# Kernel optimization log

Measured on AMD Instinct MI355X. Metric: run time of the kernel, lower is better.

The kernel has to match this reference:

```python
import jax, jax.numpy as jnp
import numpy as np

D_MODEL = 1024
NUM_HEADS = 16
D_K = D_MODEL // NUM_HEADS


def setup_inputs() -> dict:
    key = jax.random.key(0)
    ks = jax.random.split(key, 12)
    B, S = 2, 2048
    s = 1.0 / np.sqrt(D_MODEL)
    return {
        "Q": jax.random.normal(ks[0], (B, S, D_MODEL), jnp.float32),
        "K": jax.random.normal(ks[1], (B, S, D_MODEL), jnp.float32),
        "V": jax.random.normal(ks[2], (B, S, D_MODEL), jnp.float32),
        "Wq": jax.random.normal(ks[3], (D_MODEL, D_MODEL), jnp.float32) * s,
        "bq": jax.random.normal(ks[4], (D_MODEL,), jnp.float32) * s,
        "Wk": jax.random.normal(ks[5], (D_MODEL, D_MODEL), jnp.float32) * s,
        "bk": jax.random.normal(ks[6], (D_MODEL,), jnp.float32) * s,
        "Wv": jax.random.normal(ks[7], (D_MODEL, D_MODEL), jnp.float32) * s,
        "bv": jax.random.normal(ks[8], (D_MODEL,), jnp.float32) * s,
        "Wfc": jax.random.normal(ks[9], (D_MODEL, D_MODEL), jnp.float32) * s,
        "bfc": jax.random.normal(ks[10], (D_MODEL,), jnp.float32) * s,
    }


def reference(Q, K, V, Wq, bq, Wk, bk, Wv, bv, Wfc, bfc):
    B, S, _ = Q.shape
    # Linear projections, then split heads: [B, S, D] -> [B, H, S, d_k]
    def split_heads(x):
        return x.reshape(B, S, NUM_HEADS, D_K).transpose(0, 2, 1, 3)
    q = split_heads(Q @ Wq + bq)
    k = split_heads(K @ Wk + bk)
    v = split_heads(V @ Wv + bv)
    # Scaled dot-product attention (mask=None path)
    scores = jnp.einsum('bhqd,bhkd->bhqk', q, k) / jnp.sqrt(jnp.asarray(D_K, q.dtype))
    attention = jax.nn.softmax(scores, axis=-1)  # [B, H, S, S]
    context = jnp.einsum('bhqk,bhkd->bhqd', attention, v)
    context = context.transpose(0, 2, 1, 3).reshape(B, S, D_MODEL)
    output = context @ Wfc + bfc
    return output, attention
```

## Files before the change

### kernel.cpp

```cpp
#include <hip/hip_runtime.h>
#include <hip/hip_bf16.h>
#include <stdint.h>


typedef __bf16 bf16_t;
typedef __bf16 bf16x8 __attribute__((ext_vector_type(8)));
typedef float  f32x4  __attribute__((ext_vector_type(4)));

#define MFMA16(a, b, c) __builtin_amdgcn_mfma_f32_16x16x32_bf16((a), (b), (c), 0, 0, 0)

__global__ __launch_bounds__(256)
void wtrans_kernel(const float* w0, const float* w1, const float* w2,
                   const float* w3, bf16_t* wt)
{
  const float* W = blockIdx.z == 0 ? w0 : blockIdx.z == 1 ? w1
                 : blockIdx.z == 2 ? w2 : w3;
  bf16_t* O = wt + ((size_t)blockIdx.z << 20);
  __shared__ bf16_t tile[64][72];
  const int t = threadIdx.x;
  const int r0 = blockIdx.y * 64, c0 = blockIdx.x * 64;
  {
    const int r = t >> 2, cg = (t & 3) * 16;
    const float4* src = (const float4*)(W + (size_t)(r0 + r) * 1024 + c0 + cg);
#pragma unroll
    for (int u = 0; u < 4; ++u) {
      float4 f = src[u];
      tile[r][cg + u * 4 + 0] = (bf16_t)f.x;
      tile[r][cg + u * 4 + 1] = (bf16_t)f.y;
      tile[r][cg + u * 4 + 2] = (bf16_t)f.z;
      tile[r][cg + u * 4 + 3] = (bf16_t)f.w;
    }
  }
  __syncthreads();
  {
    const int c = t >> 2, rg = (t & 3) * 16;
    bf16x8 v0, v1;
#pragma unroll
    for (int u = 0; u < 8; ++u) { v0[u] = tile[rg + u][c]; v1[u] = tile[rg + 8 + u][c]; }
    bf16x8* dst = (bf16x8*)(O + (size_t)(c0 + c) * 1024 + r0 + rg);
    dst[0] = v0; dst[1] = v1;
  }
}

__global__ __launch_bounds__(256)
void vtrans_kernel(const bf16_t* vb, bf16_t* vT)
{
  __shared__ bf16_t tile[64][72];
  const int t = threadIdx.x;
  const int bh = blockIdx.y;
  const int s0 = blockIdx.x * 64;
  {
    const int s = t >> 2, dg = (t & 3) * 16;
    const bf16x8* src = (const bf16x8*)(vb + ((size_t)bh * 2048 + s0 + s) * 64 + dg);
    bf16x8 a = src[0], b = src[1];
#pragma unroll
    for (int u = 0; u < 8; ++u) { tile[s][dg + u] = a[u]; tile[s][dg + 8 + u] = b[u]; }
  }
  __syncthreads();
  {
    const int d = t >> 2, sg = (t & 3) * 16;
    bf16x8 v0, v1;
#pragma unroll
    for (int u = 0; u < 8; ++u) { v0[u] = tile[sg + u][d]; v1[u] = tile[sg + 8 + u][d]; }
    bf16x8* dst = (bf16x8*)(vT + ((size_t)bh * 64 + d) * 2048 + s0 + sg);
    dst[0] = v0; dst[1] = v1;
  }
}

template<bool A_BF16, bool OUT_SPLIT>
__global__ __launch_bounds__(256, 2)
void gemm_kernel(const void* A0, const void* A1, const void* A2,
                 const bf16_t* WTbase,
                 const float* b0, const float* b1, const float* b2,
                 void* Obase, size_t ostride)
{
  const int z = blockIdx.z;
  const void*  Aptr = z == 0 ? A0 : z == 1 ? A1 : A2;
  const float* bias = z == 0 ? b0 : z == 1 ? b1 : b2;
  const bf16_t* WT  = WTbase + ((size_t)z << 20);

  __shared__ bf16_t As[128 * 32];
  __shared__ bf16_t Bs[128 * 32];

  const int tid = threadIdx.x;
  const int lane = tid & 63, wv = tid >> 6;
  const int quad = lane >> 4, lr = lane & 15;
  const int wm = wv >> 1, wn = wv & 1;
  const int m0 = blockIdx.y * 128, n0 = blockIdx.x * 128;

  f32x4 acc[4][4];
#pragma unroll
  for (int i = 0; i < 4; ++i)
#pragma unroll
    for (int j = 0; j < 4; ++j) acc[i][j] = (f32x4){0.f, 0.f, 0.f, 0.f};

  const int srow = tid >> 1;
  const int shalf = tid & 1;
  const int swz = (srow >> 1) & 3;
  bf16_t* as0 = &As[srow * 32 + (((shalf * 2)    ) ^ swz) * 8];
  bf16_t* as1 = &As[srow * 32 + (((shalf * 2) + 1) ^ swz) * 8];
  bf16_t* bs0 = &Bs[srow * 32 + (((shalf * 2)    ) ^ swz) * 8];
  bf16_t* bs1 = &Bs[srow * 32 + (((shalf * 2) + 1) ^ swz) * 8];

  for (int kt = 0; kt < 1024; kt += 32) {
    bf16x8 av0, av1, bv0, bv1;
    if (A_BF16) {
      const bf16x8* p = (const bf16x8*)((const bf16_t*)Aptr +
                          (size_t)(m0 + srow) * 1024 + kt + shalf * 16);
      av0 = p[0]; av1 = p[1];
    } else {
      const float4* p = (const float4*)((const float*)Aptr +
                          (size_t)(m0 + srow) * 1024 + kt + shalf * 16);
      float4 f0 = p[0], f1 = p[1], f2 = p[2], f3 = p[3];
      av0[0]=(bf16_t)f0.x; av0[1]=(bf16_t)f0.y; av0[2]=(bf16_t)f0.z; av0[3]=(bf16_t)f0.w;
      av0[4]=(bf16_t)f1.x; av0[5]=(bf16_t)f1.y; av0[6]=(bf16_t)f1.z; av0[7]=(bf16_t)f1.w;
      av1[0]=(bf16_t)f2.x; av1[1]=(bf16_t)f2.y; av1[2]=(bf16_t)f2.z; av1[3]=(bf16_t)f2.w;
      av1[4]=(bf16_t)f3.x; av1[5]=(bf16_t)f3.y; av1[6]=(bf16_t)f3.z; av1[7]=(bf16_t)f3.w;
    }
    {
      const bf16x8* p = (const bf16x8*)(WT + (size_t)(n0 + srow) * 1024 + kt + shalf * 16);
      bv0 = p[0]; bv1 = p[1];
    }
    __syncthreads();
    *(bf16x8*)as0 = av0; *(bf16x8*)as1 = av1;
    *(bf16x8*)bs0 = bv0; *(bf16x8*)bs1 = bv1;
    __syncthreads();
    bf16x8 af[4], bfr[4];
#pragma unroll
    for (int i = 0; i < 4; ++i) {
      const int row = wm * 64 + i * 16 + lr;
      af[i] = *(bf16x8*)&As[row * 32 + (quad ^ ((row >> 1) & 3)) * 8];
      const int nn = wn * 64 + i * 16 + lr;
      bfr[i] = *(bf16x8*)&Bs[nn * 32 + (quad ^ ((nn >> 1) & 3)) * 8];
    }
#pragma unroll
    for (int i = 0; i < 4; ++i)
#pragma unroll
      for (int j = 0; j < 4; ++j)
        acc[i][j] = MFMA16(af[i], bfr[j], acc[i][j]);
  }

  if (OUT_SPLIT) {
    bf16_t* O = (bf16_t*)Obase + (size_t)z * ostride;
#pragma unroll
    for (int i = 0; i < 4; ++i) {
      const int mbase = m0 + wm * 64 + i * 16 + quad * 4;
#pragma unroll
      for (int j = 0; j < 4; ++j) {
        const int n = n0 + wn * 64 + j * 16 + lr;
        const float bv = bias[n];
        const int h = n >> 6, d = n & 63;
#pragma unroll
        for (int r = 0; r < 4; ++r) {
          const int m = mbase + r;
          const int b = m >> 11, s = m & 2047;
          O[((size_t)(b * 16 + h) * 2048 + s) * 64 + d] = (bf16_t)(acc[i][j][r] + bv);
        }
      }
    }
  } else {
    float* O = (float*)Obase;
#pragma unroll
    for (int i = 0; i < 4; ++i) {
      const int mbase = m0 + wm * 64 + i * 16 + quad * 4;
#pragma unroll
      for (int j = 0; j < 4; ++j) {
        const int n = n0 + wn * 64 + j * 16 + lr;
        const float bv = bias[n];
#pragma unroll
        for (int r = 0; r < 4; ++r)
          O[(size_t)(mbase + r) * 1024 + n] = acc[i][j][r] + bv;
      }
    }
  }
}

__global__ __launch_bounds__(256, 2)
void attn_kernel(const bf16_t* qb, const bf16_t* kb, const bf16_t* vT,
                 float* attn, bf16_t* ctx, float* wsum)
{
  __shared__ bf16_t P[16 * 2048];
  const int tid = threadIdx.x;
  const int lane = tid & 63, wv = tid >> 6;
  const int quad = lane >> 4, lr = lane & 15;
  const int bh = blockIdx.y;
  const int row0 = blockIdx.x * 16;
  const int blockflat = bh * 128 + blockIdx.x;

  const bf16x8* qp = (const bf16x8*)(qb + ((size_t)bh * 2048 + row0 + lr) * 64 + quad * 8);
  const bf16x8 a0 = qp[0];
  const bf16x8 a1 = qp[4];

  float sums[4] = {0.f, 0.f, 0.f, 0.f};

  for (int ct = 0; ct < 32; ++ct) {
    const int n0 = wv * 512 + ct * 16;
    const bf16x8* kp = (const bf16x8*)(kb + ((size_t)bh * 2048 + n0 + lr) * 64 + quad * 8);
    const bf16x8 b0v = kp[0];
    const bf16x8 b1v = kp[4];
    f32x4 sacc = {0.f, 0.f, 0.f, 0.f};
    sacc = MFMA16(a0, b0v, sacc);
    sacc = MFMA16(a1, b1v, sacc);
#pragma unroll
    for (int r = 0; r < 4; ++r) {
      const float p = __expf(sacc[r] * 0.125f);
      const bf16_t pb = (bf16_t)p;
      sums[r] += (float)pb;
      P[(quad * 4 + r) * 2048 + n0 + lr] = pb;
    }
  }
#pragma unroll
  for (int m = 1; m < 16; m <<= 1) {
#pragma unroll
    for (int r = 0; r < 4; ++r) sums[r] += __shfl_xor(sums[r], m, 64);
  }
  float* wsb = wsum + (size_t)blockflat * 64;
  if (lr == 0) {
#pragma unroll
    for (int r = 0; r < 4; ++r) wsb[wv * 16 + quad * 4 + r] = sums[r];
  }
  __syncthreads();

  {
    float* abase = attn + ((size_t)bh * 2048 + row0) * 2048 + tid * 8;
    for (int r = 0; r < 16; ++r) {
      const float inv = 1.0f / (wsb[r] + wsb[16 + r] + wsb[32 + r] + wsb[48 + r]);
      const bf16x8 pv = *(const bf16x8*)&P[r * 2048 + tid * 8];
      float4 o0, o1;
      o0.x = (float)pv[0] * inv; o0.y = (float)pv[1] * inv;
      o0.z = (float)pv[2] * inv; o0.w = (float)pv[3] * inv;
      o1.x = (float)pv[4] * inv; o1.y = (float)pv[5] * inv;
      o1.z = (float)pv[6] * inv; o1.w = (float)pv[7] * inv;
      float4* dst = (float4*)(abase + (size_t)r * 2048);
      dst[0] = o0; dst[1] = o1;
    }
  }

  {
    f32x4 cacc = {0.f, 0.f, 0.f, 0.f};
    const bf16_t* vbase = vT + ((size_t)bh * 64 + wv * 16 + lr) * 2048;
    for (int kt = 0; kt < 64; ++kt) {
      const bf16x8 af  = *(const bf16x8*)&P[lr * 2048 + kt * 32 + quad * 8];
      const bf16x8 bfv = *(const bf16x8*)(vbase + kt * 32 + quad * 8);
      cacc = MFMA16(af, bfv, cacc);
    }
    const int b = bh >> 4, h = bh & 15;
#pragma unroll
    for (int r = 0; r < 4; ++r) {
      const int row = quad * 4 + r;
      const float inv = 1.0f / (wsb[row] + wsb[16 + row] + wsb[32 + row] + wsb[48 + row]);
      ctx[(size_t)(b * 2048 + row0 + row) * 1024 + h * 64 + wv * 16 + lr] =
          (bf16_t)(cacc[r] * inv);
    }
  }
}

extern "C" void kernel_launch(void* const* d_in, const int* in_sizes, int n_in,
                              void* d_out, int out_size, void* d_ws, size_t ws_size,
                              hipStream_t stream)
{
  const float* Q   = (const float*)d_in[0];
  const float* K   = (const float*)d_in[1];
  const float* V   = (const float*)d_in[2];
  const float* Wq  = (const float*)d_in[3];
  const float* bq  = (const float*)d_in[4];
  const float* Wk  = (const float*)d_in[5];
  const float* bk  = (const float*)d_in[6];
  const float* Wv  = (const float*)d_in[7];
  const float* bv  = (const float*)d_in[8];
  const float* Wfc = (const float*)d_in[9];
  const float* bfc = (const float*)d_in[10];

  char* ws = (char*)d_ws;
  bf16_t* wt   = (bf16_t*)ws;
  bf16_t* qb   = (bf16_t*)(ws + (size_t)8  * (1 << 20));
  bf16_t* kb   = (bf16_t*)(ws + (size_t)16 * (1 << 20));
  bf16_t* vb   = (bf16_t*)(ws + (size_t)24 * (1 << 20));
  bf16_t* vT   = (bf16_t*)(ws + (size_t)32 * (1 << 20));
  bf16_t* ctx  = (bf16_t*)(ws + (size_t)40 * (1 << 20));
  float*  wsum = (float*) (ws + (size_t)48 * (1 << 20));

  float* out  = (float*)d_out;
  float* attn = out + (size_t)4194304;

  dim3 blk(256);
  wtrans_kernel<<<dim3(16, 16, 4), blk, 0, stream>>>(Wq, Wk, Wv, Wfc, wt);
  gemm_kernel<false, true><<<dim3(8, 32, 3), blk, 0, stream>>>(
      Q, K, V, wt, bq, bk, bv, qb, (size_t)4194304);
  vtrans_kernel<<<dim3(32, 32), blk, 0, stream>>>(vb, vT);
  attn_kernel<<<dim3(128, 32), blk, 0, stream>>>(qb, kb, vT, attn, ctx, wsum);
  gemm_kernel<true, false><<<dim3(8, 32, 1), blk, 0, stream>>>(
      ctx, ctx, ctx, wt + ((size_t)3 << 20), bfc, bfc, bfc, out, 0);
}
```

Baseline: 916.4 us.

## Remap blocks for XCD locality, swizzle P in LDS, keep row sums in shared memory

Remaps block indices in the GEMM and attention kernels so that consecutive blocks on the same XCD share K/V heads and weight tiles, aiming to improve L2 reuse. XOR-swizzles the shared-memory P buffer to reduce bank conflicts on the strided writes and reads. Moves the per-row softmax sums from global memory into shared memory, computing the reciprocal once per row instead of repeatedly. Writes the large attention matrix with nontemporal stores to avoid polluting the cache. The remapping assumes a fixed 8-way XCD round-robin and exact grid sizes.

```diff
diff --git a/kernel.cpp b/kernel.cpp
--- a/kernel.cpp
+++ b/kernel.cpp
@@ -86,7 +86,10 @@
   const int lane = tid & 63, wv = tid >> 6;
   const int quad = lane >> 4, lr = lane & 15;
   const int wm = wv >> 1, wn = wv & 1;
-  const int m0 = blockIdx.y * 128, n0 = blockIdx.x * 128;
+  const int lin2 = blockIdx.y * 8 + blockIdx.x;
+  const int idx  = lin2 >> 3;
+  const int m0 = (((lin2 & 7) << 2) + (idx >> 3)) * 128;
+  const int n0 = (idx & 7) * 128;
 
   f32x4 acc[4][4];
 #pragma unroll
@@ -177,15 +180,18 @@
 
 __global__ __launch_bounds__(256, 2)
 void attn_kernel(const bf16_t* qb, const bf16_t* kb, const bf16_t* vT,
-                 float* attn, bf16_t* ctx, float* wsum)
+                 float* attn, bf16_t* ctx)
 {
   __shared__ bf16_t P[16 * 2048];
+  __shared__ float wpart[4][16];
+  __shared__ float inv16[16];
   const int tid = threadIdx.x;
   const int lane = tid & 63, wv = tid >> 6;
   const int quad = lane >> 4, lr = lane & 15;
-  const int bh = blockIdx.y;
-  const int row0 = blockIdx.x * 16;
-  const int blockflat = bh * 128 + blockIdx.x;
+  const int lin  = blockIdx.y * 128 + blockIdx.x;
+  const int virt = ((lin & 7) << 9) + (lin >> 3);
+  const int bh   = virt >> 7;
+  const int row0 = (virt & 127) * 16;
 
   const bf16x8* qp = (const bf16x8*)(qb + ((size_t)bh * 2048 + row0 + lr) * 64 + quad * 8);
   const bf16x8 a0 = qp[0];
@@ -206,7 +212,8 @@
       const float p = __expf(sacc[r] * 0.125f);
       const bf16_t pb = (bf16_t)p;
       sums[r] += (float)pb;
-      P[(quad * 4 + r) * 2048 + n0 + lr] = pb;
+      const int prow = quad * 4 + r;
+      P[prow * 2048 + ((n0 + lr) ^ ((prow & 7) << 3))] = pb;
     }
   }
 #pragma unroll
@@ -214,25 +221,28 @@
 #pragma unroll
     for (int r = 0; r < 4; ++r) sums[r] += __shfl_xor(sums[r], m, 64);
   }
-  float* wsb = wsum + (size_t)blockflat * 64;
   if (lr == 0) {
 #pragma unroll
-    for (int r = 0; r < 4; ++r) wsb[wv * 16 + quad * 4 + r] = sums[r];
-  }
+    for (int r = 0; r < 4; ++r) wpart[wv][quad * 4 + r] = sums[r];
+  }
+  __syncthreads();
+  if (tid < 16)
+    inv16[tid] = 1.0f / (wpart[0][tid] + wpart[1][tid] + wpart[2][tid] + wpart[3][tid]);
   __syncthreads();
 
   {
     float* abase = attn + ((size_t)bh * 2048 + row0) * 2048 + tid * 8;
     for (int r = 0; r < 16; ++r) {
-      const float inv = 1.0f / (wsb[r] + wsb[16 + r] + wsb[32 + r] + wsb[48 + r]);
-      const bf16x8 pv = *(const bf16x8*)&P[r * 2048 + tid * 8];
-      float4 o0, o1;
-      o0.x = (float)pv[0] * inv; o0.y = (float)pv[1] * inv;
-      o0.z = (float)pv[2] * inv; o0.w = (float)pv[3] * inv;
-      o1.x = (float)pv[4] * inv; o1.y = (float)pv[5] * inv;
-      o1.z = (float)pv[6] * inv; o1.w = (float)pv[7] * inv;
-      float4* dst = (float4*)(abase + (size_t)r * 2048);
-      dst[0] = o0; dst[1] = o1;
+      const float inv = inv16[r];
+      const bf16x8 pv = *(const bf16x8*)&P[r * 2048 + ((tid * 8) ^ ((r & 7) << 3))];
+      f32x4 o0, o1;
+      o0[0] = (float)pv[0] * inv; o0[1] = (float)pv[1] * inv;
+      o0[2] = (float)pv[2] * inv; o0[3] = (float)pv[3] * inv;
+      o1[0] = (float)pv[4] * inv; o1[1] = (float)pv[5] * inv;
+      o1[2] = (float)pv[6] * inv; o1[3] = (float)pv[7] * inv;
+      f32x4* dst = (f32x4*)(abase + (size_t)r * 2048);
+      __builtin_nontemporal_store(o0, dst);
+      __builtin_nontemporal_store(o1, dst + 1);
     }
   }
 
@@ -240,7 +250,7 @@
     f32x4 cacc = {0.f, 0.f, 0.f, 0.f};
     const bf16_t* vbase = vT + ((size_t)bh * 64 + wv * 16 + lr) * 2048;
     for (int kt = 0; kt < 64; ++kt) {
-      const bf16x8 af  = *(const bf16x8*)&P[lr * 2048 + kt * 32 + quad * 8];
+      const bf16x8 af  = *(const bf16x8*)&P[lr * 2048 + ((kt * 32 + quad * 8) ^ ((lr & 7) << 3))];
       const bf16x8 bfv = *(const bf16x8*)(vbase + kt * 32 + quad * 8);
       cacc = MFMA16(af, bfv, cacc);
     }
@@ -248,9 +258,8 @@
 #pragma unroll
     for (int r = 0; r < 4; ++r) {
       const int row = quad * 4 + r;
-      const float inv = 1.0f / (wsb[row] + wsb[16 + row] + wsb[32 + row] + wsb[48 + row]);
       ctx[(size_t)(b * 2048 + row0 + row) * 1024 + h * 64 + wv * 16 + lr] =
-          (bf16_t)(cacc[r] * inv);
+          (bf16_t)(cacc[r] * inv16[row]);
     }
   }
 }
@@ -278,7 +287,6 @@
   bf16_t* vb   = (bf16_t*)(ws + (size_t)24 * (1 << 20));
   bf16_t* vT   = (bf16_t*)(ws + (size_t)32 * (1 << 20));
   bf16_t* ctx  = (bf16_t*)(ws + (size_t)40 * (1 << 20));
-  float*  wsum = (float*) (ws + (size_t)48 * (1 << 20));
 
   float* out  = (float*)d_out;
   float* attn = out + (size_t)4194304;
@@ -288,7 +296,7 @@
   gemm_kernel<false, true><<<dim3(8, 32, 3), blk, 0, stream>>>(
       Q, K, V, wt, bq, bk, bv, qb, (size_t)4194304);
   vtrans_kernel<<<dim3(32, 32), blk, 0, stream>>>(vb, vT);
-  attn_kernel<<<dim3(128, 32), blk, 0, stream>>>(qb, kb, vT, attn, ctx, wsum);
+  attn_kernel<<<dim3(128, 32), blk, 0, stream>>>(qb, kb, vT, attn, ctx);
   gemm_kernel<true, false><<<dim3(8, 32, 1), blk, 0, stream>>>(
       ctx, ctx, ctx, wt + ((size_t)3 << 20), bfc, bfc, bfc, out, 0);
 }
```

Measured after the change: 884.5 us. -3.5%, faster.
